# Kernel tuning notes

Measured on AMD Instinct MI355X. Metric: run time of the kernel, lower is better.

The kernel has to match this reference:

```python
import jax, jax.numpy as jnp
import numpy as np
from jax import lax

B, H = 4, 256          # batch, imsize
M1, M2 = 4096, 512     # total clusters at pooling level 1 / 2
E1, E2 = 65536, 8192   # coarsened edge counts
F = 64                 # node_feat_size (hard-coded in source)
HID = 100              # FCBlock hidden_ch


def _segment_mean(x, seg, n):
    s = jax.ops.segment_sum(x, seg, num_segments=n)
    c = jax.ops.segment_sum(jnp.ones((x.shape[0], 1), x.dtype), seg, num_segments=n)
    return s / jnp.maximum(c, 1.0)


def _fcblock(x, wi, bi, wh, bh, wo, bo):
    # FCBlock(hidden_ch=100, num_hidden_layers=3, outermost_linear=True)
    x = jax.nn.relu(x @ wi + bi)
    for k in range(wh.shape[0]):
        x = jax.nn.relu(x @ wh[k] + bh[k])
    return x @ wo + bo


def _graph_conv(x, ei, w_nei, w_self, b):
    # PyG GraphConv with aggr='mean': W_nei * mean_j x_j + W_self * x + b
    m = _segment_mean(x[ei[0]], ei[1], x.shape[0])
    return m @ w_nei + x @ w_self + b


def _render_qtr(G, feats):
    # feats: [N,20] = [centers(2), 3 channels x 6 quadratic params]
    centers = feats[:, :2]
    paras = feats[:, 2:].reshape(-1, 3, 6)
    dx = (G[:, 0] - centers[:, 0])[:, None]  # [N,1]
    dy = (G[:, 1] - centers[:, 1])[:, None]
    a, ah, aw, ahh, aww, ahw = (paras[:, :, k] for k in range(6))  # each [N,3]
    return a + ah * dx + aw * dy + ahh * dx ** 2 + aww * dy ** 2 + ahw * dx * dy


def setup_inputs() -> dict:
    key = jax.random.key(0)
    ks = iter(jax.random.split(key, 40))
    s = jnp.float32(0.05)
    d = {}
    d['img'] = jax.random.normal(next(ks), (B, H, H, 3), jnp.float32)
    d['conv_w'] = jax.random.normal(next(ks), (3, 3, 3, F), jnp.float32) * s
    d['conv_b'] = jax.random.normal(next(ks), (F,), jnp.float32) * s
    for p, din, dout in (('t1', F + 4, F), ('t2', F + 4, F), ('q', F, 18)):
        d[p + '_wi'] = jax.random.normal(next(ks), (din, HID), jnp.float32) * s
        d[p + '_bi'] = jax.random.normal(next(ks), (HID,), jnp.float32) * s
        d[p + '_wh'] = jax.random.normal(next(ks), (2, HID, HID), jnp.float32) * s
        d[p + '_bh'] = jax.random.normal(next(ks), (2, HID), jnp.float32) * s
        d[p + '_wo'] = jax.random.normal(next(ks), (HID, dout), jnp.float32) * s
        d[p + '_bo'] = jax.random.normal(next(ks), (dout,), jnp.float32) * s
    for p in ('gc1', 'gc2'):
        d[p + '_wn'] = jax.random.normal(next(ks), (F, F), jnp.float32) * s
        d[p + '_ws'] = jax.random.normal(next(ks), (F, F), jnp.float32) * s
        d[p + '_b'] = jax.random.normal(next(ks), (F,), jnp.float32) * s
    N = B * H * H
    d['cluster1'] = jax.random.randint(next(ks), (N,), 0, M1, jnp.int32)
    d['cluster2'] = jax.random.randint(next(ks), (M1,), 0, M2, jnp.int32)
    d['edges1'] = jax.random.randint(next(ks), (2, E1), 0, M1, jnp.int32)
    d['edges2'] = jax.random.randint(next(ks), (2, E2), 0, M2, jnp.int32)
    return d


def reference(img, conv_w, conv_b,
              t1_wi, t1_bi, t1_wh, t1_bh, t1_wo, t1_bo,
              t2_wi, t2_bi, t2_wh, t2_bh, t2_wo, t2_bo,
              q_wi, q_bi, q_wh, q_bh, q_wo, q_bo,
              gc1_wn, gc1_ws, gc1_b, gc2_wn, gc2_ws, gc2_b,
              cluster1, cluster2, edges1, edges2):
    b, h, w, _ = img.shape
    # RDN feature extractor stand-in: conv -> [B,H,W,F] -> flatten to pixel-nodes
    feats = lax.conv_general_dilated(img, conv_w, (1, 1), 'SAME',
                                     dimension_numbers=('NHWC', 'HWIO', 'NHWC')) + conv_b
    x = feats.reshape(-1, F)  # [N,F]
    ii, jj = jnp.meshgrid(jnp.arange(h), jnp.arange(w), indexing='ij')
    coords = jnp.stack([ii, jj], -1).reshape(-1, 2).astype(jnp.float32) / h
    coords = jnp.tile(coords, (b, 1))  # spatial_coords.repeat(batch,1)

    # ---- pooling level 1 ----
    x1 = _segment_mean(x, cluster1, M1)
    cen1 = _segment_mean(coords, cluster1, M1)
    mom1 = _segment_mean(coords ** 2, cluster1, M1)
    x1 = _fcblock(jnp.concatenate([x1, cen1, mom1], -1), t1_wi, t1_bi, t1_wh, t1_bh, t1_wo, t1_bo)
    x1 = _graph_conv(x1, edges1, gc1_wn, gc1_ws, gc1_b)

    # ---- pooling level 2 (composed cluster remap) ----
    cluster_r2 = cluster2[cluster1]  # pixel -> level-2 cluster
    x2 = _segment_mean(x1, cluster2, M2)
    cen2 = _segment_mean(coords, cluster_r2, M2)
    mom2 = _segment_mean(coords ** 2, cluster_r2, M2)
    x2 = _fcblock(jnp.concatenate([x2, cen2, mom2], -1), t2_wi, t2_bi, t2_wh, t2_bh, t2_wo, t2_bo)
    x2 = _graph_conv(x2, edges2, gc2_wn, gc2_ws, gc2_b)

    # ---- quadratic texture render per level ----
    jsf1 = jnp.concatenate([_fcblock(x1, q_wi, q_bi, q_wh, q_bh, q_wo, q_bo), cen1], -1)  # [M1,20]
    r1 = _render_qtr(coords, jsf1[cluster1]).reshape(b, h * w, 3)
    jsf2 = jnp.concatenate([_fcblock(x2, q_wi, q_bi, q_wh, q_bh, q_wo, q_bo), cen2], -1)  # [M2,20]
    r2 = _render_qtr(coords, jsf2[cluster_r2]).reshape(b, h * w, 3)
    return r1, r2, x1, x2
```

## Files before the change

### kernel.cpp

```cpp
#include <hip/hip_runtime.h>

#define NPIX 262144
#define M1C 4096
#define M2C 512
#define E1C 65536
#define E2C 8192

constexpr int IOFF_H1   = 0;
constexpr int IOFF_HC2  = IOFF_H1  + M1C;
constexpr int IOFF_HE1  = IOFF_HC2 + M2C;
constexpr int IOFF_HE2  = IOFF_HE1 + M1C;
constexpr int ZEROI_END = IOFF_HE2 + M2C;

constexpr int IOFF_ST1   = ZEROI_END;
constexpr int IOFF_CU1   = IOFF_ST1  + M1C + 1;
constexpr int IOFF_STC2  = IOFF_CU1  + M1C;
constexpr int IOFF_CUC2  = IOFF_STC2 + M2C + 1;
constexpr int IOFF_STE1  = IOFF_CUC2 + M2C;
constexpr int IOFF_CUE1  = IOFF_STE1 + M1C + 1;
constexpr int IOFF_STE2  = IOFF_CUE1 + M1C;
constexpr int IOFF_CUE2  = IOFF_STE2 + M2C + 1;
constexpr int IOFF_PLIST = IOFF_CUE2 + M2C;
constexpr int IOFF_R2L   = IOFF_PLIST + NPIX;
constexpr int IOFF_E1L   = IOFF_R2L + M1C;
constexpr int IOFF_E2L   = IOFF_E1L + E1C;
constexpr int IEND0      = IOFF_E2L + E2C;
constexpr int IEND       = (IEND0 + 3) & ~3;

constexpr int OFF_S1CR  = IEND;
constexpr int OFF_C1    = OFF_S1CR + M1C*4;
constexpr int OFF_X1FC  = OFF_C1 + M1C;
constexpr int OFF_X1    = OFF_X1FC + M1C*64;
constexpr int OFF_X2FC  = OFF_X1 + M1C*64;
constexpr int OFF_JSF1  = OFF_X2FC + M2C*64;
constexpr int OFF_JSF2  = OFF_JSF1 + M1C*20;
constexpr int OFF_PAD   = OFF_JSF2 + M2C*20;

#define PAD_ROW   774
#define PAD_BATCH 199692
#define PAD_TOT   266256

__global__ __launch_bounds__(256) void zero_ws(int* __restrict__ wsI) {
  int i = blockIdx.x*256 + threadIdx.x;
  if (i < ZEROI_END) wsI[i] = 0;
}

__global__ __launch_bounds__(256) void pad_img(
    const float* __restrict__ img, float* __restrict__ pad) {
  int idx = blockIdx.x*256 + threadIdx.x;
  if (idx >= PAD_TOT) return;
  int b = idx / 66564, r = idx - b*66564;
  int py = r / 258, px = r - py*258;
  float v0 = 0.f, v1 = 0.f, v2 = 0.f;
  int y = py - 1, x = px - 1;
  if ((unsigned)y < 256u && (unsigned)x < 256u) {
    const float* s = img + (size_t)(((b << 16) + (y << 8) + x) * 3);
    v0 = s[0]; v1 = s[1]; v2 = s[2];
  }
  float* d = pad + (size_t)idx*3;
  d[0] = v0; d[1] = v1; d[2] = v2;
}

__global__ __launch_bounds__(256) void build_hist(
    const int* __restrict__ c1, const int* __restrict__ c2,
    const int* __restrict__ e1, const int* __restrict__ e2, int* __restrict__ wsI) {
  int i = blockIdx.x*256 + threadIdx.x;
  if (i < NPIX) {
    atomicAdd(&wsI[IOFF_H1 + c1[i]], 1);
  } else if (i < NPIX + M1C) {
    atomicAdd(&wsI[IOFF_HC2 + c2[i - NPIX]], 1);
  } else if (i < NPIX + M1C + E1C) {
    int e = i - NPIX - M1C;
    atomicAdd(&wsI[IOFF_HE1 + e1[E1C + e]], 1);
  } else {
    int e = i - NPIX - M1C - E1C;
    atomicAdd(&wsI[IOFF_HE2 + e2[E2C + e]], 1);
  }
}

__global__ __launch_bounds__(1024) void scan_kernel(int* __restrict__ wsI) {
  const int* hist; int* start; int* curs; int n;
  if (blockIdx.x == 0)      { hist = wsI+IOFF_H1;  start = wsI+IOFF_ST1;  curs = wsI+IOFF_CU1;  n = M1C; }
  else if (blockIdx.x == 1) { hist = wsI+IOFF_HC2; start = wsI+IOFF_STC2; curs = wsI+IOFF_CUC2; n = M2C; }
  else if (blockIdx.x == 2) { hist = wsI+IOFF_HE1; start = wsI+IOFF_STE1; curs = wsI+IOFF_CUE1; n = M1C; }
  else                      { hist = wsI+IOFF_HE2; start = wsI+IOFF_STE2; curs = wsI+IOFF_CUE2; n = M2C; }
  __shared__ int part[1024];
  int t = threadIdx.x, base = t*4, sum = 0;
  int loc0, loc1, loc2, loc3;
  loc0 = sum; sum += (base+0 < n) ? hist[base+0] : 0;
  loc1 = sum; sum += (base+1 < n) ? hist[base+1] : 0;
  loc2 = sum; sum += (base+2 < n) ? hist[base+2] : 0;
  loc3 = sum; sum += (base+3 < n) ? hist[base+3] : 0;
  part[t] = sum;
  __syncthreads();
  for (int off = 1; off < 1024; off <<= 1) {
    int v = (t >= off) ? part[t-off] : 0;
    __syncthreads();
    part[t] += v;
    __syncthreads();
  }
  int excl = (t == 0) ? 0 : part[t-1];
  if (base+0 < n) { start[base+0] = excl+loc0; curs[base+0] = excl+loc0; }
  if (base+1 < n) { start[base+1] = excl+loc1; curs[base+1] = excl+loc1; }
  if (base+2 < n) { start[base+2] = excl+loc2; curs[base+2] = excl+loc2; }
  if (base+3 < n) { start[base+3] = excl+loc3; curs[base+3] = excl+loc3; }
  if (t == 0) start[n] = part[1023];
}

__global__ __launch_bounds__(256) void scatter_all(
    const int* __restrict__ c1, const int* __restrict__ c2,
    const int* __restrict__ e1, const int* __restrict__ e2, int* __restrict__ wsI) {
  int i = blockIdx.x*256 + threadIdx.x;
  if (i < NPIX) {
    int s = c1[i];
    int pos = atomicAdd(&wsI[IOFF_CU1 + s], 1);
    wsI[IOFF_PLIST + pos] = i;
  } else if (i < NPIX + M1C) {
    int r = i - NPIX;
    int pos = atomicAdd(&wsI[IOFF_CUC2 + c2[r]], 1);
    wsI[IOFF_R2L + pos] = r;
  } else if (i < NPIX + M1C + E1C) {
    int e = i - NPIX - M1C;
    int pos = atomicAdd(&wsI[IOFF_CUE1 + e1[E1C + e]], 1);
    wsI[IOFF_E1L + pos] = e1[e];
  } else {
    int e = i - NPIX - M1C - E1C;
    int pos = atomicAdd(&wsI[IOFF_CUE2 + e2[E2C + e]], 1);
    wsI[IOFF_E2L + pos] = e2[e];
  }
}

template<int NIN, int NOUT, int R, bool RELU>
__device__ __forceinline__ void block_layer(
    const float* __restrict__ W, const float* __restrict__ B,
    const float* __restrict__ actIn, float* __restrict__ actOut, int tid) {
  constexpr int NG  = 256 / NOUT;
  constexpr int RPT = (R + NG - 1) / NG;
  static_assert(NIN % 4 == 0, "NIN must be multiple of 4");
  int c  = tid % NOUT;
  int rg = tid / NOUT;
  if (rg < NG) {
    float acc[RPT];
    #pragma unroll
    for (int i = 0; i < RPT; ++i) acc[i] = 0.f;
    #pragma unroll 4
    for (int kc = 0; kc < NIN/4; ++kc) {
      float w0 = W[(kc*4+0)*NOUT + c];
      float w1 = W[(kc*4+1)*NOUT + c];
      float w2 = W[(kc*4+2)*NOUT + c];
      float w3 = W[(kc*4+3)*NOUT + c];
      #pragma unroll
      for (int i = 0; i < RPT; ++i) {
        int r = rg + i*NG;
        if (r < R) {
          float4 a = *reinterpret_cast<const float4*>(actIn + r*NIN + kc*4);
          acc[i] = fmaf(a.x, w0, fmaf(a.y, w1, fmaf(a.z, w2, fmaf(a.w, w3, acc[i]))));
        }
      }
    }
    float b = B[c];
    #pragma unroll
    for (int i = 0; i < RPT; ++i) {
      int r = rg + i*NG;
      if (r < R) {
        float v = acc[i] + b;
        actOut[r*NOUT + c] = RELU ? fmaxf(v, 0.f) : v;
      }
    }
  }
  __syncthreads();
}

__global__ __launch_bounds__(256) void k1_gather_t1(
    const float* __restrict__ pad, const float* __restrict__ cw, const float* __restrict__ cb,
    const int* __restrict__ start, const int* __restrict__ plist,
    const float* t1_wi, const float* t1_bi, const float* t1_wh, const float* t1_bh,
    const float* t1_wo, const float* t1_bo,
    float* __restrict__ x1fc, float* __restrict__ s1c_raw, float* __restrict__ c1f,
    float* __restrict__ jsf1) {
  int tid = threadIdx.x, wv = tid >> 6, l = tid & 63;
  int s = blockIdx.x*4 + wv;
  __shared__ __align__(16) float bufA[4*100];
  __shared__ __align__(16) float bufB[4*100];
  int p0 = start[s], p1 = start[s+1];
  int count = p1 - p0;
  float ps[27];
  #pragma unroll
  for (int k = 0; k < 27; ++k) ps[k] = 0.f;
  float sy = 0.f, sx = 0.f, syy = 0.f, sxx = 0.f;
  for (int p = p0 + l; p < p1; p += 64) {
    int n = plist[p];
    int b = n >> 16, pp = n & 65535, i = pp >> 8, j = pp & 255;
    const float* pb = pad + (size_t)b*PAD_BATCH + i*PAD_ROW + j*3;
    #pragma unroll
    for (int di = 0; di < 3; ++di) {
      const float* rp = pb + di*PAD_ROW;
      #pragma unroll
      for (int t = 0; t < 9; ++t) ps[di*9 + t] += rp[t];
    }
    float yi = i * (1.0f/256.0f), xj = j * (1.0f/256.0f);
    sy += yi; sx += xj; syy += yi*yi; sxx += xj*xj;
  }
  #pragma unroll
  for (int m = 1; m < 64; m <<= 1) {
    #pragma unroll
    for (int k = 0; k < 27; ++k) ps[k] += __shfl_xor(ps[k], m);
    sy  += __shfl_xor(sy,  m);
    sx  += __shfl_xor(sx,  m);
    syy += __shfl_xor(syy, m);
    sxx += __shfl_xor(sxx, m);
  }
  float inv = 1.0f / fmaxf((float)count, 1.0f);
  float o = cb[l];
  #pragma unroll
  for (int k = 0; k < 27; ++k) o = fmaf(ps[k]*inv, cw[k*64 + l], o);
  bufA[wv*68 + l] = count ? o : 0.f;
  if (l == 0) {
    bufA[wv*68 + 64] = sy*inv;
    bufA[wv*68 + 65] = sx*inv;
    bufA[wv*68 + 66] = syy*inv;
    bufA[wv*68 + 67] = sxx*inv;
    s1c_raw[s*4+0] = sy; s1c_raw[s*4+1] = sx;
    s1c_raw[s*4+2] = syy; s1c_raw[s*4+3] = sxx;
    jsf1[s*20 + 18] = sy*inv;
    jsf1[s*20 + 19] = sx*inv;
    c1f[s] = (float)count;
  }
  __syncthreads();
  block_layer<68,100,4,true>(t1_wi, t1_bi, bufA, bufB, tid);
  block_layer<100,100,4,true>(t1_wh, t1_bh, bufB, bufA, tid);
  block_layer<100,100,4,true>(t1_wh+10000, t1_bh+100, bufA, bufB, tid);
  block_layer<100,64,4,false>(t1_wo, t1_bo, bufB, bufA, tid);
  int r0 = blockIdx.x*4;
  for (int o2 = tid; o2 < 4*64; o2 += 256) x1fc[r0*64 + o2] = bufA[o2];
}

__device__ __forceinline__ float edge_mean(
    const int* __restrict__ elist, const float* __restrict__ xin,
    int p0, int p1, int l) {
  float a0 = 0.f, a1 = 0.f, a2 = 0.f, a3 = 0.f;
  int p = p0;
  for (; p + 3 < p1; p += 4) {
    int s0 = elist[p], s1 = elist[p+1], s2 = elist[p+2], s3 = elist[p+3];
    a0 += xin[s0*64 + l];
    a1 += xin[s1*64 + l];
    a2 += xin[s2*64 + l];
    a3 += xin[s3*64 + l];
  }
  for (; p < p1; ++p) a0 += xin[elist[p]*64 + l];
  return ((a0 + a1) + (a2 + a3)) / fmaxf((float)(p1 - p0), 1.0f);
}

__global__ __launch_bounds__(256) void k2_gc1_q(
    const int* __restrict__ startE, const int* __restrict__ elist,
    const float* __restrict__ xin,
    const float* wn, const float* wsf, const float* bias,
    const float* q_wi, const float* q_bi, const float* q_wh, const float* q_bh,
    const float* q_wo, const float* q_bo,
    float* __restrict__ x1_ws, float* __restrict__ out_f, float* __restrict__ jsf) {
  int tid = threadIdx.x, wv = tid >> 6, l = tid & 63;
  int d = blockIdx.x*4 + wv;
  __shared__ __align__(16) float bufA[4*100];
  __shared__ __align__(16) float bufB[4*100];
  __shared__ float smW[4*128];
  float* sm = smW + wv*128;
  sm[l]      = edge_mean(elist, xin, startE[d], startE[d+1], l);
  sm[64 + l] = xin[d*64 + l];
  __syncthreads();
  float o = bias[l];
  #pragma unroll 8
  for (int k = 0; k < 64; ++k)
    o += sm[k]*wn[k*64 + l] + sm[64 + k]*wsf[k*64 + l];
  x1_ws[d*64 + l] = o;
  out_f[d*64 + l] = o;
  bufA[wv*64 + l] = o;
  __syncthreads();
  block_layer<64,100,4,true>(q_wi, q_bi, bufA, bufB, tid);
  block_layer<100,100,4,true>(q_wh, q_bh, bufB, bufA, tid);
  block_layer<100,100,4,true>(q_wh+10000, q_bh+100, bufA, bufB, tid);
  block_layer<100,18,4,false>(q_wo, q_bo, bufB, bufA, tid);
  int r0 = blockIdx.x*4;
  for (int o2 = tid; o2 < 4*18; o2 += 256) {
    int r = o2 / 18, c = o2 - r*18;
    jsf[(r0+r)*20 + c] = bufA[o2];
  }
}

__global__ __launch_bounds__(256) void k3_pool_t2(
    const int* __restrict__ startc2, const int* __restrict__ r2list,
    const float* __restrict__ x1, const float* __restrict__ s1c_raw, const float* __restrict__ c1f,
    const float* t2_wi, const float* t2_bi, const float* t2_wh, const float* t2_bh,
    const float* t2_wo, const float* t2_bo,
    float* __restrict__ x2fc, float* __restrict__ jsf2) {
  int tid = threadIdx.x, wv = tid >> 6, l = tid & 63;
  int s2 = blockIdx.x*4 + wv;
  __shared__ __align__(16) float bufA[4*100];
  __shared__ __align__(16) float bufB[4*100];
  int p0 = startc2[s2], p1 = startc2[s2+1];
  int k = l & 3;
  float acc = 0.f, sc = 0.f, cnt = 0.f;
  for (int p = p0; p < p1; ++p) {
    int r = r2list[p];
    acc += x1[r*64 + l];
    sc  += s1c_raw[r*4 + k];
    cnt += c1f[r];
  }
  float invr = 1.0f / fmaxf((float)(p1 - p0), 1.0f);
  bufA[wv*68 + l] = acc * invr;
  if (l < 4) {
    float mean = sc / fmaxf(cnt, 1.0f);
    bufA[wv*68 + 64 + l] = mean;
    if (l == 0) jsf2[s2*20 + 18] = mean;
    if (l == 1) jsf2[s2*20 + 19] = mean;
  }
  __syncthreads();
  block_layer<68,100,4,true>(t2_wi, t2_bi, bufA, bufB, tid);
  block_layer<100,100,4,true>(t2_wh, t2_bh, bufB, bufA, tid);
  block_layer<100,100,4,true>(t2_wh+10000, t2_bh+100, bufA, bufB, tid);
  block_layer<100,64,4,false>(t2_wo, t2_bo, bufB, bufA, tid);
  int r0 = blockIdx.x*4;
  for (int o2 = tid; o2 < 4*64; o2 += 256) x2fc[r0*64 + o2] = bufA[o2];
}

__global__ __launch_bounds__(256) void k4_gc2_q(
    const int* __restrict__ startE, const int* __restrict__ elist,
    const float* __restrict__ xin,
    const float* wn, const float* wsf, const float* bias,
    const float* q_wi, const float* q_bi, const float* q_wh, const float* q_bh,
    const float* q_wo, const float* q_bo,
    float* __restrict__ out_f, float* __restrict__ jsf2) {
  int tid = threadIdx.x, wv = tid >> 6, l = tid & 63;
  int d = blockIdx.x*4 + wv;
  __shared__ __align__(16) float bufA[4*100];
  __shared__ __align__(16) float bufB[4*100];
  __shared__ float smW[4*128];
  float* sm = smW + wv*128;
  sm[l]      = edge_mean(elist, xin, startE[d], startE[d+1], l);
  sm[64 + l] = xin[d*64 + l];
  __syncthreads();
  float o = bias[l];
  #pragma unroll 8
  for (int k = 0; k < 64; ++k)
    o += sm[k]*wn[k*64 + l] + sm[64 + k]*wsf[k*64 + l];
  out_f[d*64 + l] = o;
  bufA[wv*64 + l] = o;
  __syncthreads();
  block_layer<64,100,4,true>(q_wi, q_bi, bufA, bufB, tid);
  block_layer<100,100,4,true>(q_wh, q_bh, bufB, bufA, tid);
  block_layer<100,100,4,true>(q_wh+10000, q_bh+100, bufA, bufB, tid);
  block_layer<100,18,4,false>(q_wo, q_bo, bufB, bufA, tid);
  int r0 = blockIdx.x*4;
  for (int o2 = tid; o2 < 4*18; o2 += 256) {
    int r = o2 / 18, c = o2 - r*18;
    jsf2[(r0+r)*20 + c] = bufA[o2];
  }
}

__global__ __launch_bounds__(256) void render_kernel(
    const int* __restrict__ cluster1, const int* __restrict__ cluster2,
    const float* __restrict__ jsf1, const float* __restrict__ jsf2,
    float* __restrict__ r1, float* __restrict__ r2) {
  int n = blockIdx.x*256 + threadIdx.x;
  int p = n & 65535, i = p >> 8, j = p & 255;
  float gy = i * (1.0f/256.0f), gx = j * (1.0f/256.0f);
  int s = cluster1[n];
  {
    const float4* f4 = reinterpret_cast<const float4*>(jsf1 + s*20);
    float4 v0 = f4[0], v1 = f4[1], v2 = f4[2], v3 = f4[3], v4 = f4[4];
    float dx = gy - v0.x, dy = gx - v0.y;
    float dxx = dx*dx, dyy = dy*dy, dxy = dx*dy;
    r1[n*3 + 0] = v0.z + v0.w*dx + v1.x*dy + v1.y*dxx + v1.z*dyy + v1.w*dxy;
    r1[n*3 + 1] = v2.x + v2.y*dx + v2.z*dy + v2.w*dxx + v3.x*dyy + v3.y*dxy;
    r1[n*3 + 2] = v3.z + v3.w*dx + v4.x*dy + v4.y*dxx + v4.z*dyy + v4.w*dxy;
  }
  int s2 = cluster2[s];
  {
    const float4* f4 = reinterpret_cast<const float4*>(jsf2 + s2*20);
    float4 v0 = f4[0], v1 = f4[1], v2 = f4[2], v3 = f4[3], v4 = f4[4];
    float dx = gy - v0.x, dy = gx - v0.y;
    float dxx = dx*dx, dyy = dy*dy, dxy = dx*dy;
    r2[n*3 + 0] = v0.z + v0.w*dx + v1.x*dy + v1.y*dxx + v1.z*dyy + v1.w*dxy;
    r2[n*3 + 1] = v2.x + v2.y*dx + v2.z*dy + v2.w*dxx + v3.x*dyy + v3.y*dxy;
    r2[n*3 + 2] = v3.z + v3.w*dx + v4.x*dy + v4.y*dxx + v4.z*dyy + v4.w*dxy;
  }
}

extern "C" void kernel_launch(void* const* d_in, const int* in_sizes, int n_in,
                              void* d_out, int out_size, void* d_ws, size_t ws_size,
                              hipStream_t stream) {
  const float* img    = (const float*)d_in[0];
  const float* conv_w = (const float*)d_in[1];
  const float* conv_b = (const float*)d_in[2];
  const float* t1_wi = (const float*)d_in[3];  const float* t1_bi = (const float*)d_in[4];
  const float* t1_wh = (const float*)d_in[5];  const float* t1_bh = (const float*)d_in[6];
  const float* t1_wo = (const float*)d_in[7];  const float* t1_bo = (const float*)d_in[8];
  const float* t2_wi = (const float*)d_in[9];  const float* t2_bi = (const float*)d_in[10];
  const float* t2_wh = (const float*)d_in[11]; const float* t2_bh = (const float*)d_in[12];
  const float* t2_wo = (const float*)d_in[13]; const float* t2_bo = (const float*)d_in[14];
  const float* q_wi  = (const float*)d_in[15]; const float* q_bi  = (const float*)d_in[16];
  const float* q_wh  = (const float*)d_in[17]; const float* q_bh  = (const float*)d_in[18];
  const float* q_wo  = (const float*)d_in[19]; const float* q_bo  = (const float*)d_in[20];
  const float* gc1_wn = (const float*)d_in[21]; const float* gc1_ws = (const float*)d_in[22];
  const float* gc1_b  = (const float*)d_in[23];
  const float* gc2_wn = (const float*)d_in[24]; const float* gc2_ws = (const float*)d_in[25];
  const float* gc2_b  = (const float*)d_in[26];
  const int* cluster1 = (const int*)d_in[27];
  const int* cluster2 = (const int*)d_in[28];
  const int* edges1   = (const int*)d_in[29];
  const int* edges2   = (const int*)d_in[30];

  float* ws = (float*)d_ws;
  int*   wsI = (int*)d_ws;
  float* out  = (float*)d_out;
  float* o_r1 = out;
  float* o_r2 = out + 786432;
  float* o_x1 = out + 1572864;
  float* o_x2 = out + 1835008;

  zero_ws<<<(ZEROI_END + 255)/256, 256, 0, stream>>>(wsI);
  pad_img<<<(PAD_TOT + 255)/256, 256, 0, stream>>>(img, ws + OFF_PAD);

  constexpr int TOTW = NPIX + M1C + E1C + E2C;
  build_hist<<<TOTW/256, 256, 0, stream>>>(cluster1, cluster2, edges1, edges2, wsI);
  scan_kernel<<<4, 1024, 0, stream>>>(wsI);
  scatter_all<<<TOTW/256, 256, 0, stream>>>(cluster1, cluster2, edges1, edges2, wsI);

  k1_gather_t1<<<M1C/4, 256, 0, stream>>>(ws + OFF_PAD, conv_w, conv_b,
      wsI+IOFF_ST1, wsI+IOFF_PLIST,
      t1_wi, t1_bi, t1_wh, t1_bh, t1_wo, t1_bo,
      ws+OFF_X1FC, ws+OFF_S1CR, ws+OFF_C1, ws+OFF_JSF1);

  k2_gc1_q<<<M1C/4, 256, 0, stream>>>(wsI+IOFF_STE1, wsI+IOFF_E1L, ws+OFF_X1FC,
      gc1_wn, gc1_ws, gc1_b,
      q_wi, q_bi, q_wh, q_bh, q_wo, q_bo,
      ws+OFF_X1, o_x1, ws+OFF_JSF1);

  k3_pool_t2<<<M2C/4, 256, 0, stream>>>(wsI+IOFF_STC2, wsI+IOFF_R2L,
      ws+OFF_X1, ws+OFF_S1CR, ws+OFF_C1,
      t2_wi, t2_bi, t2_wh, t2_bh, t2_wo, t2_bo,
      ws+OFF_X2FC, ws+OFF_JSF2);

  k4_gc2_q<<<M2C/4, 256, 0, stream>>>(wsI+IOFF_STE2, wsI+IOFF_E2L, ws+OFF_X2FC,
      gc2_wn, gc2_ws, gc2_b,
      q_wi, q_bi, q_wh, q_bh, q_wo, q_bo,
      o_x2, ws+OFF_JSF2);

  render_kernel<<<NPIX/256, 256, 0, stream>>>(cluster1, cluster2, ws+OFF_JSF1, ws+OFF_JSF2, o_r1, o_r2);
}
```

Baseline: 169.9 us.

## Process eight clusters per block in level-1 kernels and fuse zeroing into padding

k1_gather_t1 and k2_gc1_q now have each wave handle two cluster rows, so a block covers eight rows. The FCBlock layers therefore load each weight matrix once per eight rows instead of once per four, which halves global weight traffic per row. The workspace zeroing kernel is folded into the image padding kernel, removing one launch. The cost is half as many blocks (512 on the GPU), so there is less parallelism for the latency-bound gather phase. In k2 the per-wave shared scratch is also reused without a block barrier, which relies on each wave's shared-memory accesses staying in order.

After: 167.9 us. About the same (-1.1%).

```diff
diff --git a/kernel.cpp b/kernel.cpp
--- a/kernel.cpp
+++ b/kernel.cpp
@@ -40,14 +40,10 @@
 #define PAD_BATCH 199692
 #define PAD_TOT   266256
 
-__global__ __launch_bounds__(256) void zero_ws(int* __restrict__ wsI) {
-  int i = blockIdx.x*256 + threadIdx.x;
-  if (i < ZEROI_END) wsI[i] = 0;
-}
-
-__global__ __launch_bounds__(256) void pad_img(
-    const float* __restrict__ img, float* __restrict__ pad) {
+__global__ __launch_bounds__(256) void prep(
+    const float* __restrict__ img, float* __restrict__ pad, int* __restrict__ wsI) {
   int idx = blockIdx.x*256 + threadIdx.x;
+  if (idx < ZEROI_END) wsI[idx] = 0;
   if (idx >= PAD_TOT) return;
   int b = idx / 66564, r = idx - b*66564;
   int py = r / 258, px = r - py*258;
@@ -179,60 +175,64 @@
     float* __restrict__ x1fc, float* __restrict__ s1c_raw, float* __restrict__ c1f,
     float* __restrict__ jsf1) {
   int tid = threadIdx.x, wv = tid >> 6, l = tid & 63;
-  int s = blockIdx.x*4 + wv;
-  __shared__ __align__(16) float bufA[4*100];
-  __shared__ __align__(16) float bufB[4*100];
-  int p0 = start[s], p1 = start[s+1];
-  int count = p1 - p0;
-  float ps[27];
+  __shared__ __align__(16) float bufA[8*100];
+  __shared__ __align__(16) float bufB[8*100];
   #pragma unroll
-  for (int k = 0; k < 27; ++k) ps[k] = 0.f;
-  float sy = 0.f, sx = 0.f, syy = 0.f, sxx = 0.f;
-  for (int p = p0 + l; p < p1; p += 64) {
-    int n = plist[p];
-    int b = n >> 16, pp = n & 65535, i = pp >> 8, j = pp & 255;
-    const float* pb = pad + (size_t)b*PAD_BATCH + i*PAD_ROW + j*3;
+  for (int cc = 0; cc < 2; ++cc) {
+    int row = wv*2 + cc;
+    int s = blockIdx.x*8 + row;
+    int p0 = start[s], p1 = start[s+1];
+    int count = p1 - p0;
+    float ps[27];
     #pragma unroll
-    for (int di = 0; di < 3; ++di) {
-      const float* rp = pb + di*PAD_ROW;
+    for (int k = 0; k < 27; ++k) ps[k] = 0.f;
+    float sy = 0.f, sx = 0.f, syy = 0.f, sxx = 0.f;
+    for (int p = p0 + l; p < p1; p += 64) {
+      int n = plist[p];
+      int b = n >> 16, pp = n & 65535, i = pp >> 8, j = pp & 255;
+      const float* pb = pad + (size_t)b*PAD_BATCH + i*PAD_ROW + j*3;
       #pragma unroll
-      for (int t = 0; t < 9; ++t) ps[di*9 + t] += rp[t];
+      for (int di = 0; di < 3; ++di) {
+        const float* rp = pb + di*PAD_ROW;
+        #pragma unroll
+        for (int t = 0; t < 9; ++t) ps[di*9 + t] += rp[t];
+      }
+      float yi = i * (1.0f/256.0f), xj = j * (1.0f/256.0f);
+      sy += yi; sx += xj; syy += yi*yi; sxx += xj*xj;
     }
-    float yi = i * (1.0f/256.0f), xj = j * (1.0f/256.0f);
-    sy += yi; sx += xj; syy += yi*yi; sxx += xj*xj;
-  }
-  #pragma unroll
-  for (int m = 1; m < 64; m <<= 1) {
     #pragma unroll
-    for (int k = 0; k < 27; ++k) ps[k] += __shfl_xor(ps[k], m);
-    sy  += __shfl_xor(sy,  m);
-    sx  += __shfl_xor(sx,  m);
-    syy += __shfl_xor(syy, m);
-    sxx += __shfl_xor(sxx, m);
-  }
-  float inv = 1.0f / fmaxf((float)count, 1.0f);
-  float o = cb[l];
-  #pragma unroll
-  for (int k = 0; k < 27; ++k) o = fmaf(ps[k]*inv, cw[k*64 + l], o);
-  bufA[wv*68 + l] = count ? o : 0.f;
-  if (l == 0) {
-    bufA[wv*68 + 64] = sy*inv;
-    bufA[wv*68 + 65] = sx*inv;
-    bufA[wv*68 + 66] = syy*inv;
-    bufA[wv*68 + 67] = sxx*inv;
-    s1c_raw[s*4+0] = sy; s1c_raw[s*4+1] = sx;
-    s1c_raw[s*4+2] = syy; s1c_raw[s*4+3] = sxx;
-    jsf1[s*20 + 18] = sy*inv;
-    jsf1[s*20 + 19] = sx*inv;
-    c1f[s] = (float)count;
-  }
-  __syncthreads();
-  block_layer<68,100,4,true>(t1_wi, t1_bi, bufA, bufB, tid);
-  block_layer<100,100,4,true>(t1_wh, t1_bh, bufB, bufA, tid);
-  block_layer<100,100,4,true>(t1_wh+10000, t1_bh+100, bufA, bufB, tid);
-  block_layer<100,64,4,false>(t1_wo, t1_bo, bufB, bufA, tid);
-  int r0 = blockIdx.x*4;
-  for (int o2 = tid; o2 < 4*64; o2 += 256) x1fc[r0*64 + o2] = bufA[o2];
+    for (int m = 1; m < 64; m <<= 1) {
+      #pragma unroll
+      for (int k = 0; k < 27; ++k) ps[k] += __shfl_xor(ps[k], m);
+      sy  += __shfl_xor(sy,  m);
+      sx  += __shfl_xor(sx,  m);
+      syy += __shfl_xor(syy, m);
+      sxx += __shfl_xor(sxx, m);
+    }
+    float inv = 1.0f / fmaxf((float)count, 1.0f);
+    float o = cb[l];
+    #pragma unroll
+    for (int k = 0; k < 27; ++k) o = fmaf(ps[k]*inv, cw[k*64 + l], o);
+    bufA[row*68 + l] = count ? o : 0.f;
+    if (l == 0) {
+      bufA[row*68 + 64] = sy*inv;
+      bufA[row*68 + 65] = sx*inv;
+      bufA[row*68 + 66] = syy*inv;
+      bufA[row*68 + 67] = sxx*inv;
+      s1c_raw[s*4+0] = sy; s1c_raw[s*4+1] = sx;
+      s1c_raw[s*4+2] = syy; s1c_raw[s*4+3] = sxx;
+      jsf1[s*20 + 18] = sy*inv;
+      jsf1[s*20 + 19] = sx*inv;
+      c1f[s] = (float)count;
+    }
+  }
+  __syncthreads();
+  block_layer<68,100,8,true>(t1_wi, t1_bi, bufA, bufB, tid);
+  block_layer<100,100,8,true>(t1_wh, t1_bh, bufB, bufA, tid);
+  block_layer<100,100,8,true>(t1_wh+10000, t1_bh+100, bufA, bufB, tid);
+  block_layer<100,64,8,false>(t1_wo, t1_bo, bufB, bufA, tid);
+  int r0 = blockIdx.x*8;
+  for (int o2 = tid; o2 < 8*64; o2 += 256) x1fc[r0*64 + o2] = bufA[o2];
 }
 
 __device__ __forceinline__ float edge_mean(
@@ -259,28 +259,31 @@
     const float* q_wo, const float* q_bo,
     float* __restrict__ x1_ws, float* __restrict__ out_f, float* __restrict__ jsf) {
   int tid = threadIdx.x, wv = tid >> 6, l = tid & 63;
-  int d = blockIdx.x*4 + wv;
-  __shared__ __align__(16) float bufA[4*100];
-  __shared__ __align__(16) float bufB[4*100];
+  __shared__ __align__(16) float bufA[8*100];
+  __shared__ __align__(16) float bufB[8*100];
   __shared__ float smW[4*128];
   float* sm = smW + wv*128;
-  sm[l]      = edge_mean(elist, xin, startE[d], startE[d+1], l);
-  sm[64 + l] = xin[d*64 + l];
-  __syncthreads();
-  float o = bias[l];
-  #pragma unroll 8
-  for (int k = 0; k < 64; ++k)
-    o += sm[k]*wn[k*64 + l] + sm[64 + k]*wsf[k*64 + l];
-  x1_ws[d*64 + l] = o;
-  out_f[d*64 + l] = o;
-  bufA[wv*64 + l] = o;
-  __syncthreads();
-  block_layer<64,100,4,true>(q_wi, q_bi, bufA, bufB, tid);
-  block_layer<100,100,4,true>(q_wh, q_bh, bufB, bufA, tid);
-  block_layer<100,100,4,true>(q_wh+10000, q_bh+100, bufA, bufB, tid);
-  block_layer<100,18,4,false>(q_wo, q_bo, bufB, bufA, tid);
-  int r0 = blockIdx.x*4;
-  for (int o2 = tid; o2 < 4*18; o2 += 256) {
+  #pragma unroll
+  for (int cc = 0; cc < 2; ++cc) {
+    int row = wv*2 + cc;
+    int d = blockIdx.x*8 + row;
+    sm[l]      = edge_mean(elist, xin, startE[d], startE[d+1], l);
+    sm[64 + l] = xin[d*64 + l];
+    float o = bias[l];
+    #pragma unroll 8
+    for (int k = 0; k < 64; ++k)
+      o += sm[k]*wn[k*64 + l] + sm[64 + k]*wsf[k*64 + l];
+    x1_ws[d*64 + l] = o;
+    out_f[d*64 + l] = o;
+    bufA[row*64 + l] = o;
+  }
+  __syncthreads();
+  block_layer<64,100,8,true>(q_wi, q_bi, bufA, bufB, tid);
+  block_layer<100,100,8,true>(q_wh, q_bh, bufB, bufA, tid);
+  block_layer<100,100,8,true>(q_wh+10000, q_bh+100, bufA, bufB, tid);
+  block_layer<100,18,8,false>(q_wo, q_bo, bufB, bufA, tid);
+  int r0 = blockIdx.x*8;
+  for (int o2 = tid; o2 < 8*18; o2 += 256) {
     int r = o2 / 18, c = o2 - r*18;
     jsf[(r0+r)*20 + c] = bufA[o2];
   }
@@ -417,20 +420,19 @@
   float* o_x1 = out + 1572864;
   float* o_x2 = out + 1835008;
 
-  zero_ws<<<(ZEROI_END + 255)/256, 256, 0, stream>>>(wsI);
-  pad_img<<<(PAD_TOT + 255)/256, 256, 0, stream>>>(img, ws + OFF_PAD);
+  prep<<<(PAD_TOT + 255)/256, 256, 0, stream>>>(img, ws + OFF_PAD, wsI);
 
   constexpr int TOTW = NPIX + M1C + E1C + E2C;
   build_hist<<<TOTW/256, 256, 0, stream>>>(cluster1, cluster2, edges1, edges2, wsI);
   scan_kernel<<<4, 1024, 0, stream>>>(wsI);
   scatter_all<<<TOTW/256, 256, 0, stream>>>(cluster1, cluster2, edges1, edges2, wsI);
 
-  k1_gather_t1<<<M1C/4, 256, 0, stream>>>(ws + OFF_PAD, conv_w, conv_b,
+  k1_gather_t1<<<M1C/8, 256, 0, stream>>>(ws + OFF_PAD, conv_w, conv_b,
       wsI+IOFF_ST1, wsI+IOFF_PLIST,
       t1_wi, t1_bi, t1_wh, t1_bh, t1_wo, t1_bo,
       ws+OFF_X1FC, ws+OFF_S1CR, ws+OFF_C1, ws+OFF_JSF1);
 
-  k2_gc1_q<<<M1C/4, 256, 0, stream>>>(wsI+IOFF_STE1, wsI+IOFF_E1L, ws+OFF_X1FC,
+  k2_gc1_q<<<M1C/8, 256, 0, stream>>>(wsI+IOFF_STE1, wsI+IOFF_E1L, ws+OFF_X1FC,
       gc1_wn, gc1_ws, gc1_b,
       q_wi, q_bi, q_wh, q_bh, q_wo, q_bo,
       ws+OFF_X1, o_x1, ws+OFF_JSF1);
```
